# Performance work log

Measured on AMD Instinct MI355X. Metric: run time of the kernel, lower is better.

## Reference

```python
import jax, jax.numpy as jnp
import numpy as np

B, T, NX, NY, E, BS = 2, 8, 32, 32, 768, 64
NB = E // BS            # 12 blocks
YM = NY // 2 + 1        # 17 rfft y modes
KM = 12                 # kept_modes (hardcoded in source)
XS = slice(YM - KM, YM + KM)  # slice(5,29) on the x-mode axis (faithful quirk: bounds use y_modes)
LAM = 0.01


def _ln(x, g, b, eps=1e-5):
    m = x.mean(-1, keepdims=True)
    v = ((x - m) ** 2).mean(-1, keepdims=True)
    return (x - m) / jnp.sqrt(v + eps) * g + b


def _softshrink(x, lam=LAM):
    return jnp.where(x > lam, x - lam, jnp.where(x < -lam, x + lam, jnp.zeros((), x.dtype)))


def setup_inputs() -> dict:
    key = jax.random.key(0)
    ks = jax.random.split(key, 8)
    s = 0.02
    return {
        'input': jax.random.normal(ks[0], (B, T, NX * NY, E), jnp.float32),
        'w1': s * jax.random.normal(ks[1], (2, NB, BS, BS), jnp.float32),
        'b1': s * jax.random.normal(ks[2], (2, 1, 1, 1, NB, BS), jnp.float32),
        'w2': s * jax.random.normal(ks[3], (2, NB, BS, BS), jnp.float32),
        'b2': s * jax.random.normal(ks[4], (2, 1, 1, 1, NB, BS), jnp.float32),
        'ln1_g': jnp.ones((E,), jnp.float32),
        'ln1_b': jnp.zeros((E,), jnp.float32),
        'ln2_g': jnp.ones((E,), jnp.float32),
        'ln2_b': jnp.zeros((E,), jnp.float32),
        'mw1': s * jax.random.normal(ks[5], (E, 4 * E), jnp.float32),
        'mb1': jnp.zeros((4 * E,), jnp.float32),
        'mw2': s * jax.random.normal(ks[6], (4 * E, E), jnp.float32),
        'mb2': jnp.zeros((E,), jnp.float32),
    }


def reference(input, w1, b1, w2, b2, ln1_g, ln1_b, ln2_g, ln2_b, mw1, mb1, mw2, mb2):
    residual = input
    h = _ln(input, ln1_g, ln1_b)                       # ln1
    r = h.reshape(B, T, NX, NY, E)
    fc = jnp.fft.rfft2(r, axes=(2, 3), norm='ortho')   # (B,T,NX,YM,E) complex
    fc = fc.reshape(B, T, NX, YM, NB, BS)
    fr = fc.real[:, :, XS, :KM]                        # (B,T,24,12,NB,BS)
    fi = fc.imag[:, :, XS, :KM]
    op = 'btxyni,nio->btxyno'
    o1r = jax.nn.gelu(jnp.einsum(op, fr, w1[0]) - jnp.einsum(op, fi, w1[1]) + b1[0], approximate=False)
    o1i = jax.nn.gelu(jnp.einsum(op, fi, w1[0]) + jnp.einsum(op, fr, w1[1]) + b1[1], approximate=False)
    o2r = jnp.einsum(op, o1r, w2[0]) - jnp.einsum(op, o1i, w2[1]) + b2[0]
    o2i = jnp.einsum(op, o1i, w2[0]) + jnp.einsum(op, o1r, w2[1]) + b2[1]
    out_r = jnp.zeros(fc.shape, jnp.float32).at[:, :, XS, :KM].set(_softshrink(o2r))
    out_i = jnp.zeros(fc.shape, jnp.float32).at[:, :, XS, :KM].set(_softshrink(o2i))
    oc = (out_r + 1j * out_i).reshape(B, T, NX, YM, E)
    spat = jnp.fft.irfft2(oc, s=(NX, NY), axes=(2, 3), norm='ortho').reshape(B, T, NX * NY, E)
    out = spat + h + residual                          # faithful: adds ln1(input) and original input
    res2 = out
    out = _ln(out, ln2_g, ln2_b)                       # ln2
    out = jax.nn.gelu(out @ mw1 + mb1, approximate=False) @ mw2 + mb2
    return out + res2
```

## Files before the change

### kernel.cpp

```cpp
#include <hip/hip_runtime.h>
#include <hip/hip_bf16.h>
#include <math.h>

typedef __bf16 bf16;
typedef __bf16 bf16x8 __attribute__((ext_vector_type(8)));
typedef float f32x4 __attribute__((ext_vector_type(4)));
typedef short short8 __attribute__((ext_vector_type(8)));

#define E_ 768
#define S_ 1024
#define BT_ 16
#define KM_ 12
#define KX_ 24
#define NPOS_ 4608
#define NB_ 12
#define LDST 40

__device__ __forceinline__ float gelu_exact(float x) {
    return 0.5f * x * (1.0f + erff(x * 0.70710678118654752f));
}

__device__ __forceinline__ bf16x8 neg8(bf16x8 v) {
    short8 s;
    __builtin_memcpy(&s, &v, 16);
    s ^= (short)0x8000;
    bf16x8 r;
    __builtin_memcpy(&r, &s, 16);
    return r;
}

__global__ __launch_bounds__(256) void k_ln_stats(const float* __restrict__ x,
                                                  float* __restrict__ mu, float* __restrict__ rs) {
    int row = blockIdx.x;
    int t = threadIdx.x;
    const float* xr = x + (size_t)row * E_;
    float v0 = xr[t], v1 = xr[t + 256], v2 = xr[t + 512];
    float s = v0 + v1 + v2;
    float ss = v0 * v0 + v1 * v1 + v2 * v2;
    for (int off = 32; off > 0; off >>= 1) {
        s  += __shfl_xor(s, off);
        ss += __shfl_xor(ss, off);
    }
    __shared__ float ls[4], lss[4];
    int w = t >> 6, l = t & 63;
    if (l == 0) { ls[w] = s; lss[w] = ss; }
    __syncthreads();
    if (t == 0) {
        s  = ls[0] + ls[1] + ls[2] + ls[3];
        ss = lss[0] + lss[1] + lss[2] + lss[3];
        float m = s * (1.0f / E_);
        float var = ss * (1.0f / E_) - m * m;
        mu[row] = m;
        rs[row] = rsqrtf(var + 1e-5f);
    }
}

__global__ __launch_bounds__(256) void k_ln2(const float* __restrict__ x,
                                             const float* __restrict__ g,
                                             const float* __restrict__ b,
                                             bf16* __restrict__ out) {
    int row = blockIdx.x;
    int t = threadIdx.x;
    const float* xr = x + (size_t)row * E_;
    float v0 = xr[t], v1 = xr[t + 256], v2 = xr[t + 512];
    float s = v0 + v1 + v2;
    float ss = v0 * v0 + v1 * v1 + v2 * v2;
    for (int off = 32; off > 0; off >>= 1) {
        s  += __shfl_xor(s, off);
        ss += __shfl_xor(ss, off);
    }
    __shared__ float ls[4], lss[4];
    int w = t >> 6, l = t & 63;
    if (l == 0) { ls[w] = s; lss[w] = ss; }
    __syncthreads();
    s  = ls[0] + ls[1] + ls[2] + ls[3];
    ss = lss[0] + lss[1] + lss[2] + lss[3];
    float m = s * (1.0f / E_);
    float var = ss * (1.0f / E_) - m * m;
    float r = rsqrtf(var + 1e-5f);
    #pragma unroll
    for (int q = 0; q < 3; q++) {
        int e = t + q * 256;
        float v = (q == 0) ? v0 : ((q == 1) ? v1 : v2);
        out[(size_t)row * E_ + e] = (bf16)((v - m) * r * g[e] + b[e]);
    }
}

__global__ __launch_bounds__(256) void k_dft_y(const float* __restrict__ inp,
                                               const float* __restrict__ mu, const float* __restrict__ rs,
                                               const float* __restrict__ g, const float* __restrict__ bb,
                                               float* __restrict__ gre, float* __restrict__ gim) {
    int bid = blockIdx.x;
    int ec = bid % 3, x = (bid / 3) % 32, bt = bid / 96;
    int t = threadIdx.x;
    __shared__ float tile[32 * 256];
    __shared__ float c32[32], s32[32];
    if (t < 32) { float a = 6.28318530717958647692f * t / 32.0f; c32[t] = cosf(a); s32[t] = sinf(a); }
    int e = ec * 256 + t;
    float gv = g[e], bv = bb[e];
    int row0 = bt * S_ + x * 32;
    const float* base = inp + (size_t)row0 * E_ + e;
    for (int y = 0; y < 32; y++) {
        float m = mu[row0 + y], r = rs[row0 + y];
        tile[y * 256 + t] = (base[(size_t)y * E_] - m) * r * gv + bv;
    }
    __syncthreads();
    for (int ky = 0; ky < KM_; ky++) {
        float re = 0.f, im = 0.f;
        for (int y = 0; y < 32; y++) {
            int j = (ky * y) & 31;
            float v = tile[y * 256 + t];
            re += v * c32[j];
            im -= v * s32[j];
        }
        size_t o = ((size_t)((bt * 32 + x) * KM_ + ky)) * E_ + e;
        gre[o] = re; gim[o] = im;
    }
}

__global__ __launch_bounds__(256) void k_dft_x(const float* __restrict__ gre, const float* __restrict__ gim,
                                               float* __restrict__ fr, float* __restrict__ fi) {
    int bid = blockIdx.x;
    int ec = bid % 3, ky = (bid / 3) % KM_, bt = bid / (3 * KM_);
    int t = threadIdx.x;
    __shared__ float lre[16 * 256];
    __shared__ float lim[16 * 256];
    __shared__ float c32[32], s32[32];
    if (t < 32) { float a = 6.28318530717958647692f * t / 32.0f; c32[t] = cosf(a); s32[t] = sinf(a); }
    float ar[KX_], ai[KX_];
    #pragma unroll
    for (int k = 0; k < KX_; k++) { ar[k] = 0.f; ai[k] = 0.f; }
    for (int half = 0; half < 2; half++) {
        __syncthreads();
        for (int xi = 0; xi < 16; xi++) {
            int x = half * 16 + xi;
            size_t o = ((size_t)((bt * 32 + x) * KM_ + ky)) * E_ + ec * 256 + t;
            lre[xi * 256 + t] = gre[o];
            lim[xi * 256 + t] = gim[o];
        }
        __syncthreads();
        for (int kxi = 0; kxi < KX_; kxi++) {
            int kx = kxi + 5;
            float re = 0.f, im = 0.f;
            #pragma unroll
            for (int xi = 0; xi < 16; xi++) {
                int j = (kx * (half * 16 + xi)) & 31;
                float c = c32[j], s = s32[j];
                float gr = lre[xi * 256 + t], gi = lim[xi * 256 + t];
                re += gr * c + gi * s;
                im += gi * c - gr * s;
            }
            ar[kxi] += re; ai[kxi] += im;
        }
    }
    #pragma unroll
    for (int kxi = 0; kxi < KX_; kxi++) {
        size_t p = (size_t)(bt * KX_ + kxi) * KM_ + ky;
        fr[p * E_ + ec * 256 + t] = ar[kxi] * (1.0f / 32.0f);
        fi[p * E_ + ec * 256 + t] = ai[kxi] * (1.0f / 32.0f);
    }
}

__global__ __launch_bounds__(256) void k_blockmlp(float* fr, float* fi,
                                                  const float* __restrict__ w1, const float* __restrict__ b1,
                                                  const float* __restrict__ w2, const float* __restrict__ b2) {
    int n = blockIdx.x / 36;
    int p0 = (blockIdx.x % 36) * 128;
    int t = threadIdx.x;
    __shared__ __align__(16) bf16 lXr[128 * 72];
    __shared__ __align__(16) bf16 lXi[128 * 72];
    __shared__ __align__(16) bf16 lW1a[64 * 72];
    __shared__ __align__(16) bf16 lW1b[64 * 72];
    __shared__ __align__(16) bf16 lW2a[64 * 72];
    __shared__ __align__(16) bf16 lW2b[64 * 72];

    {
        int o = t & 63, iq = t >> 6;
        const float* s1a = w1 + (size_t)n * 4096;
        const float* s1b = w1 + (size_t)(NB_ + n) * 4096;
        const float* s2a = w2 + (size_t)n * 4096;
        const float* s2b = w2 + (size_t)(NB_ + n) * 4096;
        #pragma unroll
        for (int ii = 0; ii < 16; ii++) {
            int i = iq * 16 + ii;
            lW1a[o * 72 + i] = (bf16)s1a[i * 64 + o];
            lW1b[o * 72 + i] = (bf16)s1b[i * 64 + o];
            lW2a[o * 72 + i] = (bf16)s2a[i * 64 + o];
            lW2b[o * 72 + i] = (bf16)s2b[i * 64 + o];
        }
    }
    {
        int ch4 = (t & 15) * 4, prow = t >> 4;
        #pragma unroll
        for (int rep = 0; rep < 8; rep++) {
            int p = rep * 16 + prow;
            size_t ga = (size_t)(p0 + p) * E_ + n * 64 + ch4;
            float4 vr = *(const float4*)&fr[ga];
            float4 vi = *(const float4*)&fi[ga];
            bf16 br[4] = {(bf16)vr.x, (bf16)vr.y, (bf16)vr.z, (bf16)vr.w};
            bf16 bi[4] = {(bf16)vi.x, (bf16)vi.y, (bf16)vi.z, (bf16)vi.w};
            *(uint2*)&lXr[p * 72 + ch4] = *(uint2*)br;
            *(uint2*)&lXi[p * 72 + ch4] = *(uint2*)bi;
        }
    }
    int w = t >> 6, l = t & 63, lr = l & 15, lq = l >> 4;
    float bias1r[4], bias1i[4], bias2r[4], bias2i[4];
    #pragma unroll
    for (int ni = 0; ni < 4; ni++) {
        int o = n * 64 + ni * 16 + lr;
        bias1r[ni] = b1[o]; bias1i[ni] = b1[NB_ * 64 + o];
        bias2r[ni] = b2[o]; bias2i[ni] = b2[NB_ * 64 + o];
    }
    __syncthreads();

    f32x4 a1r[2][4], a1i[2][4];
    #pragma unroll
    for (int mt = 0; mt < 2; mt++)
        #pragma unroll
        for (int ni = 0; ni < 4; ni++) { a1r[mt][ni] = (f32x4){0,0,0,0}; a1i[mt][ni] = (f32x4){0,0,0,0}; }
    #pragma unroll
    for (int ks = 0; ks < 2; ks++) {
        int k0 = ks * 32;
        bf16x8 xr[2], xi[2], xin[2];
        #pragma unroll
        for (int mt = 0; mt < 2; mt++) {
            int row = w * 32 + mt * 16 + lr;
            xr[mt]  = *(bf16x8*)&lXr[row * 72 + k0 + lq * 8];
            xi[mt]  = *(bf16x8*)&lXi[row * 72 + k0 + lq * 8];
            xin[mt] = neg8(xi[mt]);
        }
        #pragma unroll
        for (int ni = 0; ni < 4; ni++) {
            bf16x8 ba = *(bf16x8*)&lW1a[(ni * 16 + lr) * 72 + k0 + lq * 8];
            bf16x8 bb = *(bf16x8*)&lW1b[(ni * 16 + lr) * 72 + k0 + lq * 8];
            #pragma unroll
            for (int mt = 0; mt < 2; mt++) {
                a1r[mt][ni] = __builtin_amdgcn_mfma_f32_16x16x32_bf16(xr[mt],  ba, a1r[mt][ni], 0, 0, 0);
                a1r[mt][ni] = __builtin_amdgcn_mfma_f32_16x16x32_bf16(xin[mt], bb, a1r[mt][ni], 0, 0, 0);
                a1i[mt][ni] = __builtin_amdgcn_mfma_f32_16x16x32_bf16(xi[mt],  ba, a1i[mt][ni], 0, 0, 0);
                a1i[mt][ni] = __builtin_amdgcn_mfma_f32_16x16x32_bf16(xr[mt],  bb, a1i[mt][ni], 0, 0, 0);
            }
        }
    }
    #pragma unroll
    for (int mt = 0; mt < 2; mt++)
        #pragma unroll
        for (int ni = 0; ni < 4; ni++) {
            int o = ni * 16 + lr;
            #pragma unroll
            for (int r = 0; r < 4; r++) {
                int row = w * 32 + mt * 16 + lq * 4 + r;
                lXr[row * 72 + o] = (bf16)gelu_exact(a1r[mt][ni][r] + bias1r[ni]);
                lXi[row * 72 + o] = (bf16)gelu_exact(a1i[mt][ni][r] + bias1i[ni]);
            }
        }

    f32x4 a2r[2][4], a2i[2][4];
    #pragma unroll
    for (int mt = 0; mt < 2; mt++)
        #pragma unroll
        for (int ni = 0; ni < 4; ni++) { a2r[mt][ni] = (f32x4){0,0,0,0}; a2i[mt][ni] = (f32x4){0,0,0,0}; }
    #pragma unroll
    for (int ks = 0; ks < 2; ks++) {
        int k0 = ks * 32;
        bf16x8 xr[2], xi[2], xin[2];
        #pragma unroll
        for (int mt = 0; mt < 2; mt++) {
            int row = w * 32 + mt * 16 + lr;
            xr[mt]  = *(bf16x8*)&lXr[row * 72 + k0 + lq * 8];
            xi[mt]  = *(bf16x8*)&lXi[row * 72 + k0 + lq * 8];
            xin[mt] = neg8(xi[mt]);
        }
        #pragma unroll
        for (int ni = 0; ni < 4; ni++) {
            bf16x8 ba = *(bf16x8*)&lW2a[(ni * 16 + lr) * 72 + k0 + lq * 8];
            bf16x8 bb = *(bf16x8*)&lW2b[(ni * 16 + lr) * 72 + k0 + lq * 8];
            #pragma unroll
            for (int mt = 0; mt < 2; mt++) {
                a2r[mt][ni] = __builtin_amdgcn_mfma_f32_16x16x32_bf16(xr[mt],  ba, a2r[mt][ni], 0, 0, 0);
                a2r[mt][ni] = __builtin_amdgcn_mfma_f32_16x16x32_bf16(xin[mt], bb, a2r[mt][ni], 0, 0, 0);
                a2i[mt][ni] = __builtin_amdgcn_mfma_f32_16x16x32_bf16(xi[mt],  ba, a2i[mt][ni], 0, 0, 0);
                a2i[mt][ni] = __builtin_amdgcn_mfma_f32_16x16x32_bf16(xr[mt],  bb, a2i[mt][ni], 0, 0, 0);
            }
        }
    }
    #pragma unroll
    for (int mt = 0; mt < 2; mt++)
        #pragma unroll
        for (int ni = 0; ni < 4; ni++) {
            int o = ni * 16 + lr;
            #pragma unroll
            for (int r = 0; r < 4; r++) {
                int row = w * 32 + mt * 16 + lq * 4 + r;
                float vr = a2r[mt][ni][r] + bias2r[ni];
                float vi = a2i[mt][ni][r] + bias2i[ni];
                vr = (vr > 0.01f) ? vr - 0.01f : ((vr < -0.01f) ? vr + 0.01f : 0.0f);
                vi = (vi > 0.01f) ? vi - 0.01f : ((vi < -0.01f) ? vi + 0.01f : 0.0f);
                size_t ga = (size_t)(p0 + row) * E_ + n * 64 + o;
                fr[ga] = vr;
                fi[ga] = vi;
            }
        }
}

__global__ __launch_bounds__(256) void k_idft_x(const float* __restrict__ pr_, const float* __restrict__ pi_,
                                                float* __restrict__ zre, float* __restrict__ zim) {
    int bid = blockIdx.x;
    int ec = bid % 3, ky = (bid / 3) % KM_, bt = bid / (3 * KM_);
    int t = threadIdx.x;
    __shared__ float lre[KX_ * 256], lim[KX_ * 256];
    __shared__ float c32[32], s32[32];
    if (t < 32) { float a = 6.28318530717958647692f * t / 32.0f; c32[t] = cosf(a); s32[t] = sinf(a); }
    for (int kxi = 0; kxi < KX_; kxi++) {
        size_t p = (size_t)(bt * KX_ + kxi) * KM_ + ky;
        lre[kxi * 256 + t] = pr_[p * E_ + ec * 256 + t];
        lim[kxi * 256 + t] = pi_[p * E_ + ec * 256 + t];
    }
    __syncthreads();
    for (int x = 0; x < 32; x++) {
        float re = 0.f, im = 0.f;
        for (int kxi = 0; kxi < KX_; kxi++) {
            int kx = kxi + 5;
            int j = (kx * x) & 31;
            float c = c32[j], s = s32[j];
            float pr = lre[kxi * 256 + t], pi = lim[kxi * 256 + t];
            re += pr * c - pi * s;
            im += pr * s + pi * c;
        }
        size_t zo = ((size_t)((bt * 32 + x) * KM_ + ky)) * E_ + ec * 256 + t;
        zre[zo] = re; zim[zo] = im;
    }
}

__global__ __launch_bounds__(256) void k_idft_y_res(const float* __restrict__ zre, const float* __restrict__ zim,
                                                    const float* __restrict__ inp,
                                                    const float* __restrict__ mu, const float* __restrict__ rs,
                                                    const float* __restrict__ g, const float* __restrict__ bb,
                                                    float* __restrict__ out) {
    int bid = blockIdx.x;
    int ec = bid % 3, x = (bid / 3) % 32, bt = bid / 96;
    int t = threadIdx.x;
    __shared__ float lre[KM_ * 256], lim[KM_ * 256];
    __shared__ float c32[32], s32[32];
    if (t < 32) { float a = 6.28318530717958647692f * t / 32.0f; c32[t] = cosf(a); s32[t] = sinf(a); }
    for (int ky = 0; ky < KM_; ky++) {
        size_t zo = ((size_t)((bt * 32 + x) * KM_ + ky)) * E_ + ec * 256 + t;
        lre[ky * 256 + t] = zre[zo];
        lim[ky * 256 + t] = zim[zo];
    }
    __syncthreads();
    int e = ec * 256 + t;
    float gv = g[e], bv = bb[e];
    int row0 = bt * S_ + x * 32;
    for (int y = 0; y < 32; y++) {
        float v = lre[t];
        for (int ky = 1; ky < KM_; ky++) {
            int j = (ky * y) & 31;
            v += 2.0f * (lre[ky * 256 + t] * c32[j] - lim[ky * 256 + t] * s32[j]);
        }
        v *= (1.0f / 32.0f);
        size_t o = (size_t)(row0 + y) * E_ + e;
        float iv = inp[o];
        float m = mu[row0 + y], r = rs[row0 + y];
        out[o] = v + ((iv - m) * r * gv + bv) + iv;
    }
}

__global__ void k_transpose_cast(const float* __restrict__ src, bf16* __restrict__ dst, int R, int C) {
    __shared__ float tile[32][33];
    int c0 = blockIdx.x * 32, r0 = blockIdx.y * 32;
    int tx = threadIdx.x, ty = threadIdx.y;
    #pragma unroll
    for (int j = 0; j < 32; j += 8)
        tile[ty + j][tx] = src[(size_t)(r0 + ty + j) * C + c0 + tx];
    __syncthreads();
    #pragma unroll
    for (int j = 0; j < 32; j += 8)
        dst[(size_t)(c0 + ty + j) * R + r0 + tx] = (bf16)tile[tx][ty + j];
}

template<bool FUSE_GELU>
__global__ __launch_bounds__(256) void k_gemm(const bf16* __restrict__ A, const bf16* __restrict__ Bt,
                                              const float* __restrict__ bias, int M, int N, int K,
                                              bf16* __restrict__ outb, float* __restrict__ outf) {
    __shared__ __align__(16) bf16 lA[128 * LDST];
    __shared__ __align__(16) bf16 lB[128 * LDST];
    int t = threadIdx.x;
    int m0 = blockIdx.x * 128, n0 = blockIdx.y * 128;
    int w = t >> 6, l = t & 63;
    int wm = (w & 1) * 64, wn = (w >> 1) * 64;
    int lr = l & 15, lq = l >> 4;
    f32x4 acc[4][4];
    #pragma unroll
    for (int i = 0; i < 4; i++)
        #pragma unroll
        for (int j = 0; j < 4; j++)
            acc[i][j] = (f32x4){0.f, 0.f, 0.f, 0.f};
    int r0 = t >> 2;
    int ks = t & 3;
    const bf16* pa  = A  + (size_t)(m0 + r0) * K + ks * 8;
    const bf16* pa2 = pa + (size_t)64 * K;
    const bf16* pb  = Bt + (size_t)(n0 + r0) * K + ks * 8;
    const bf16* pb2 = pb + (size_t)64 * K;
    uint4 ra0 = *(const uint4*)pa;
    uint4 ra1 = *(const uint4*)pa2;
    uint4 rb0 = *(const uint4*)pb;
    uint4 rb1 = *(const uint4*)pb2;
    int nk = K / 32;
    for (int kt = 0; kt < nk; kt++) {
        *(uint4*)&lA[r0 * LDST + ks * 8] = ra0;
        *(uint4*)&lA[(r0 + 64) * LDST + ks * 8] = ra1;
        *(uint4*)&lB[r0 * LDST + ks * 8] = rb0;
        *(uint4*)&lB[(r0 + 64) * LDST + ks * 8] = rb1;
        __syncthreads();
        if (kt + 1 < nk) {
            int ko = (kt + 1) * 32;
            ra0 = *(const uint4*)(pa + ko);
            ra1 = *(const uint4*)(pa2 + ko);
            rb0 = *(const uint4*)(pb + ko);
            rb1 = *(const uint4*)(pb2 + ko);
        }
        bf16x8 af[4], bfv[4];
        #pragma unroll
        for (int mi = 0; mi < 4; mi++) af[mi]  = *(bf16x8*)&lA[(wm + mi * 16 + lr) * LDST + lq * 8];
        #pragma unroll
        for (int ni = 0; ni < 4; ni++) bfv[ni] = *(bf16x8*)&lB[(wn + ni * 16 + lr) * LDST + lq * 8];
        #pragma unroll
        for (int mi = 0; mi < 4; mi++)
            #pragma unroll
            for (int ni = 0; ni < 4; ni++)
                acc[mi][ni] = __builtin_amdgcn_mfma_f32_16x16x32_bf16(af[mi], bfv[ni], acc[mi][ni], 0, 0, 0);
        __syncthreads();
    }
    #pragma unroll
    for (int mi = 0; mi < 4; mi++) {
        #pragma unroll
        for (int ni = 0; ni < 4; ni++) {
            int col = n0 + wn + ni * 16 + lr;
            float bv = bias[col];
            #pragma unroll
            for (int r = 0; r < 4; r++) {
                int row = m0 + wm + mi * 16 + lq * 4 + r;
                float v = acc[mi][ni][r] + bv;
                if (FUSE_GELU) {
                    outb[(size_t)row * N + col] = (bf16)gelu_exact(v);
                } else {
                    size_t oo = (size_t)row * N + col;
                    outf[oo] = v + outf[oo];
                }
            }
        }
    }
}

extern "C" void kernel_launch(void* const* d_in, const int* in_sizes, int n_in,
                              void* d_out, int out_size, void* d_ws, size_t ws_size,
                              hipStream_t stream) {
    const float* input = (const float*)d_in[0];
    const float* w1    = (const float*)d_in[1];
    const float* b1    = (const float*)d_in[2];
    const float* w2    = (const float*)d_in[3];
    const float* b2    = (const float*)d_in[4];
    const float* ln1g  = (const float*)d_in[5];
    const float* ln1b  = (const float*)d_in[6];
    const float* ln2g  = (const float*)d_in[7];
    const float* ln2b  = (const float*)d_in[8];
    const float* mw1   = (const float*)d_in[9];
    const float* mb1   = (const float*)d_in[10];
    const float* mw2   = (const float*)d_in[11];
    const float* mb2   = (const float*)d_in[12];
    float* out = (float*)d_out;

    float* ws = (float*)d_ws;
    float* mu  = ws;
    float* rs  = ws + 16384;
    const size_t BASE = 32768;
    float* gre = ws + BASE;
    float* gim = gre + 4718592;
    float* fr  = ws + BASE + 2 * 4718592;
    float* fi  = fr + 3538944;
    bf16* lnA = (bf16*)(ws + BASE);
    bf16* w1T = (bf16*)(ws + BASE + 6291456);
    bf16* w2T = (bf16*)(ws + BASE + 7471104);
    bf16* mid = (bf16*)(ws + BASE + 8650752);

    const size_t fixed_fl = BASE + 6291456 + 1179648 + 1179648;
    size_t avail_fl = ws_size / 4;
    int nch;
    if      (avail_fl >= fixed_fl + 25165824) nch = 1;
    else if (avail_fl >= fixed_fl + 12582912) nch = 2;
    else                                      nch = 4;
    int MC = 16384 / nch;

    k_ln_stats<<<16384, 256, 0, stream>>>(input, mu, rs);
    k_dft_y<<<BT_ * 32 * 3, 256, 0, stream>>>(input, mu, rs, ln1g, ln1b, gre, gim);
    k_dft_x<<<BT_ * KM_ * 3, 256, 0, stream>>>(gre, gim, fr, fi);
    k_blockmlp<<<NB_ * 36, 256, 0, stream>>>(fr, fi, w1, b1, w2, b2);
    k_idft_x<<<BT_ * KM_ * 3, 256, 0, stream>>>(fr, fi, gre, gim);
    k_idft_y_res<<<BT_ * 32 * 3, 256, 0, stream>>>(gre, gim, input, mu, rs, ln1g, ln1b, out);
    k_ln2<<<16384, 256, 0, stream>>>(out, ln2g, ln2b, lnA);
    k_transpose_cast<<<dim3(3072 / 32, 768 / 32), dim3(32, 8), 0, stream>>>(mw1, w1T, 768, 3072);
    k_transpose_cast<<<dim3(768 / 32, 3072 / 32), dim3(32, 8), 0, stream>>>(mw2, w2T, 3072, 768);
    for (int c = 0; c < nch; c++) {
        const bf16* aC = lnA + (size_t)c * MC * 768;
        float* oC = out + (size_t)c * MC * 768;
        k_gemm<true><<<dim3(MC / 128, 24), 256, 0, stream>>>(aC, w1T, mb1, MC, 3072, 768, mid, nullptr);
        k_gemm<false><<<dim3(MC / 128, 6), 256, 0, stream>>>(mid, w2T, mb2, MC, 768, 3072, nullptr, oC);
    }
}
```

Baseline: 542.7 us.

## Store spectral intermediates in bf16 and swizzle GEMM shared-memory tiles

Converts the intermediate buffers passed between the DFT, block-MLP and inverse-DFT kernels from fp32 to bf16, halving the memory traffic of these bandwidth-bound stages. The block MLP now loads bf16 directly without conversion. Separately, the GEMM LDS layout drops the padded stride of 40 for an XOR-swizzled stride of 32, aimed at avoiding bank conflicts with less shared memory. Storing intermediates in bf16 adds rounding error to the spectral path.

```diff
diff --git a/kernel.cpp b/kernel.cpp
--- a/kernel.cpp
+++ b/kernel.cpp
@@ -14,10 +14,13 @@
 #define KX_ 24
 #define NPOS_ 4608
 #define NB_ 12
-#define LDST 40
 
 __device__ __forceinline__ float gelu_exact(float x) {
     return 0.5f * x * (1.0f + erff(x * 0.70710678118654752f));
+}
+
+__device__ __forceinline__ int lidx(int row, int chunk) {
+    return row * 32 + ((chunk ^ ((row >> 1) & 3)) * 8);
 }
 
 __device__ __forceinline__ bf16x8 neg8(bf16x8 v) {
@@ -89,7 +92,7 @@
 __global__ __launch_bounds__(256) void k_dft_y(const float* __restrict__ inp,
                                                const float* __restrict__ mu, const float* __restrict__ rs,
                                                const float* __restrict__ g, const float* __restrict__ bb,
-                                               float* __restrict__ gre, float* __restrict__ gim) {
+                                               bf16* __restrict__ gre, bf16* __restrict__ gim) {
     int bid = blockIdx.x;
     int ec = bid % 3, x = (bid / 3) % 32, bt = bid / 96;
     int t = threadIdx.x;
@@ -114,12 +117,12 @@
             im -= v * s32[j];
         }
         size_t o = ((size_t)((bt * 32 + x) * KM_ + ky)) * E_ + e;
-        gre[o] = re; gim[o] = im;
-    }
-}
-
-__global__ __launch_bounds__(256) void k_dft_x(const float* __restrict__ gre, const float* __restrict__ gim,
-                                               float* __restrict__ fr, float* __restrict__ fi) {
+        gre[o] = (bf16)re; gim[o] = (bf16)im;
+    }
+}
+
+__global__ __launch_bounds__(256) void k_dft_x(const bf16* __restrict__ gre, const bf16* __restrict__ gim,
+                                               bf16* __restrict__ fr, bf16* __restrict__ fi) {
     int bid = blockIdx.x;
     int ec = bid % 3, ky = (bid / 3) % KM_, bt = bid / (3 * KM_);
     int t = threadIdx.x;
@@ -135,8 +138,8 @@
         for (int xi = 0; xi < 16; xi++) {
             int x = half * 16 + xi;
             size_t o = ((size_t)((bt * 32 + x) * KM_ + ky)) * E_ + ec * 256 + t;
-            lre[xi * 256 + t] = gre[o];
-            lim[xi * 256 + t] = gim[o];
+            lre[xi * 256 + t] = (float)gre[o];
+            lim[xi * 256 + t] = (float)gim[o];
         }
         __syncthreads();
         for (int kxi = 0; kxi < KX_; kxi++) {
@@ -156,12 +159,12 @@
     #pragma unroll
     for (int kxi = 0; kxi < KX_; kxi++) {
         size_t p = (size_t)(bt * KX_ + kxi) * KM_ + ky;
-        fr[p * E_ + ec * 256 + t] = ar[kxi] * (1.0f / 32.0f);
-        fi[p * E_ + ec * 256 + t] = ai[kxi] * (1.0f / 32.0f);
-    }
-}
-
-__global__ __launch_bounds__(256) void k_blockmlp(float* fr, float* fi,
+        fr[p * E_ + ec * 256 + t] = (bf16)(ar[kxi] * (1.0f / 32.0f));
+        fi[p * E_ + ec * 256 + t] = (bf16)(ai[kxi] * (1.0f / 32.0f));
+    }
+}
+
+__global__ __launch_bounds__(256) void k_blockmlp(bf16* fr, bf16* fi,
                                                   const float* __restrict__ w1, const float* __restrict__ b1,
                                                   const float* __restrict__ w2, const float* __restrict__ b2) {
     int n = blockIdx.x / 36;
@@ -195,12 +198,8 @@
         for (int rep = 0; rep < 8; rep++) {
             int p = rep * 16 + prow;
             size_t ga = (size_t)(p0 + p) * E_ + n * 64 + ch4;
-            float4 vr = *(const float4*)&fr[ga];
-            float4 vi = *(const float4*)&fi[ga];
-            bf16 br[4] = {(bf16)vr.x, (bf16)vr.y, (bf16)vr.z, (bf16)vr.w};
-            bf16 bi[4] = {(bf16)vi.x, (bf16)vi.y, (bf16)vi.z, (bf16)vi.w};
-            *(uint2*)&lXr[p * 72 + ch4] = *(uint2*)br;
-            *(uint2*)&lXi[p * 72 + ch4] = *(uint2*)bi;
+            *(uint2*)&lXr[p * 72 + ch4] = *(const uint2*)&fr[ga];
+            *(uint2*)&lXi[p * 72 + ch4] = *(const uint2*)&fi[ga];
         }
     }
     int w = t >> 6, l = t & 63, lr = l & 15, lq = l >> 4;
@@ -297,14 +296,14 @@
                 vr = (vr > 0.01f) ? vr - 0.01f : ((vr < -0.01f) ? vr + 0.01f : 0.0f);
                 vi = (vi > 0.01f) ? vi - 0.01f : ((vi < -0.01f) ? vi + 0.01f : 0.0f);
                 size_t ga = (size_t)(p0 + row) * E_ + n * 64 + o;
-                fr[ga] = vr;
-                fi[ga] = vi;
+                fr[ga] = (bf16)vr;
+                fi[ga] = (bf16)vi;
             }
         }
 }
 
-__global__ __launch_bounds__(256) void k_idft_x(const float* __restrict__ pr_, const float* __restrict__ pi_,
-                                                float* __restrict__ zre, float* __restrict__ zim) {
+__global__ __launch_bounds__(256) void k_idft_x(const bf16* __restrict__ pr_, const bf16* __restrict__ pi_,
+                                                bf16* __restrict__ zre, bf16* __restrict__ zim) {
     int bid = blockIdx.x;
     int ec = bid % 3, ky = (bid / 3) % KM_, bt = bid / (3 * KM_);
     int t = threadIdx.x;
@@ -313,8 +312,8 @@
     if (t < 32) { float a = 6.28318530717958647692f * t / 32.0f; c32[t] = cosf(a); s32[t] = sinf(a); }
     for (int kxi = 0; kxi < KX_; kxi++) {
         size_t p = (size_t)(bt * KX_ + kxi) * KM_ + ky;
-        lre[kxi * 256 + t] = pr_[p * E_ + ec * 256 + t];
-        lim[kxi * 256 + t] = pi_[p * E_ + ec * 256 + t];
+        lre[kxi * 256 + t] = (float)pr_[p * E_ + ec * 256 + t];
+        lim[kxi * 256 + t] = (float)pi_[p * E_ + ec * 256 + t];
     }
     __syncthreads();
     for (int x = 0; x < 32; x++) {
@@ -328,11 +327,11 @@
             im += pr * s + pi * c;
         }
         size_t zo = ((size_t)((bt * 32 + x) * KM_ + ky)) * E_ + ec * 256 + t;
-        zre[zo] = re; zim[zo] = im;
-    }
-}
-
-__global__ __launch_bounds__(256) void k_idft_y_res(const float* __restrict__ zre, const float* __restrict__ zim,
+        zre[zo] = (bf16)re; zim[zo] = (bf16)im;
+    }
+}
+
+__global__ __launch_bounds__(256) void k_idft_y_res(const bf16* __restrict__ zre, const bf16* __restrict__ zim,
                                                     const float* __restrict__ inp,
                                                     const float* __restrict__ mu, const float* __restrict__ rs,
                                                     const float* __restrict__ g, const float* __restrict__ bb,
@@ -345,8 +344,8 @@
     if (t < 32) { float a = 6.28318530717958647692f * t / 32.0f; c32[t] = cosf(a); s32[t] = sinf(a); }
     for (int ky = 0; ky < KM_; ky++) {
         size_t zo = ((size_t)((bt * 32 + x) * KM_ + ky)) * E_ + ec * 256 + t;
-        lre[ky * 256 + t] = zre[zo];
-        lim[ky * 256 + t] = zim[zo];
+        lre[ky * 256 + t] = (float)zre[zo];
+        lim[ky * 256 + t] = (float)zim[zo];
     }
     __syncthreads();
     int e = ec * 256 + t;
@@ -383,8 +382,8 @@
 __global__ __launch_bounds__(256) void k_gemm(const bf16* __restrict__ A, const bf16* __restrict__ Bt,
                                               const float* __restrict__ bias, int M, int N, int K,
                                               bf16* __restrict__ outb, float* __restrict__ outf) {
-    __shared__ __align__(16) bf16 lA[128 * LDST];
-    __shared__ __align__(16) bf16 lB[128 * LDST];
+    __shared__ __align__(16) bf16 lA[128 * 32];
+    __shared__ __align__(16) bf16 lB[128 * 32];
     int t = threadIdx.x;
     int m0 = blockIdx.x * 128, n0 = blockIdx.y * 128;
     int w = t >> 6, l = t & 63;
@@ -408,10 +407,10 @@
     uint4 rb1 = *(const uint4*)pb2;
     int nk = K / 32;
     for (int kt = 0; kt < nk; kt++) {
-        *(uint4*)&lA[r0 * LDST + ks * 8] = ra0;
-        *(uint4*)&lA[(r0 + 64) * LDST + ks * 8] = ra1;
-        *(uint4*)&lB[r0 * LDST + ks * 8] = rb0;
-        *(uint4*)&lB[(r0 + 64) * LDST + ks * 8] = rb1;
+        *(uint4*)&lA[lidx(r0, ks)] = ra0;
+        *(uint4*)&lA[lidx(r0 + 64, ks)] = ra1;
+        *(uint4*)&lB[lidx(r0, ks)] = rb0;
+        *(uint4*)&lB[lidx(r0 + 64, ks)] = rb1;
         __syncthreads();
         if (kt + 1 < nk) {
             int ko = (kt + 1) * 32;
@@ -422,9 +421,9 @@
         }
         bf16x8 af[4], bfv[4];
         #pragma unroll
-        for (int mi = 0; mi < 4; mi++) af[mi]  = *(bf16x8*)&lA[(wm + mi * 16 + lr) * LDST + lq * 8];
-        #pragma unroll
-        for (int ni = 0; ni < 4; ni++) bfv[ni] = *(bf16x8*)&lB[(wn + ni * 16 + lr) * LDST + lq * 8];
+        for (int mi = 0; mi < 4; mi++) af[mi]  = *(bf16x8*)&lA[lidx(wm + mi * 16 + lr, lq)];
+        #pragma unroll
+        for (int ni = 0; ni < 4; ni++) bfv[ni] = *(bf16x8*)&lB[lidx(wn + ni * 16 + lr, lq)];
         #pragma unroll
         for (int mi = 0; mi < 4; mi++)
             #pragma unroll
@@ -475,10 +474,11 @@
     float* mu  = ws;
     float* rs  = ws + 16384;
     const size_t BASE = 32768;
-    float* gre = ws + BASE;
-    float* gim = gre + 4718592;
-    float* fr  = ws + BASE + 2 * 4718592;
-    float* fi  = fr + 3538944;
+    bf16* p1  = (bf16*)(ws + BASE);
+    bf16* gre = p1;
+    bf16* gim = gre + 4718592;
+    bf16* fr  = gim + 4718592;
+    bf16* fi  = fr + 3538944;
     bf16* lnA = (bf16*)(ws + BASE);
     bf16* w1T = (bf16*)(ws + BASE + 6291456);
     bf16* w2T = (bf16*)(ws + BASE + 7471104);
```

Measured after the change: 549.3 us. About the same (+1.2%).
